# Optimization experiments

Hardware: AMD Instinct MI355X
Metric: run time of the kernel (lower is better)

Reference implementation:

```python
import jax, jax.numpy as jnp
import numpy as np

B, N, D = 4, 1024, 1024
H = 16
DH = D // H  # 64
DROPOUT_P = 0.5


def setup_inputs() -> dict:
    key = jax.random.key(0)
    ks = jax.random.split(key, 6)
    query = jax.random.normal(ks[0], (B, N, D), dtype=jnp.float32)
    key_t = jax.random.normal(ks[1], (B, N, D), dtype=jnp.float32)
    value = jax.random.normal(ks[2], (B, N, D), dtype=jnp.float32)
    # torch Linear(D, 3D): weight [3D, D], bias [3D]
    W_qkv = jax.random.normal(ks[3], (3 * D, D), dtype=jnp.float32) * (1.0 / np.sqrt(D))
    b_qkv = jax.random.normal(ks[4], (3 * D,), dtype=jnp.float32) * 0.01
    # inverted dropout mask: keep_prob = 1 - p, kept entries scaled by 1/keep
    keep = 1.0 - DROPOUT_P
    drop_mask = (jax.random.uniform(ks[5], (B * H, N, N)) < keep).astype(jnp.float32) / keep
    return {"query": query, "key": key_t, "value": value,
            "W_qkv": W_qkv, "b_qkv": b_qkv, "drop_mask": drop_mask}


def _split_heads(t):
    # 'b n (h d) -> (b h) n d'
    b, n, _ = t.shape
    return t.reshape(b, n, H, DH).transpose(0, 2, 1, 3).reshape(b * H, n, DH)


def reference(query, key, value, W_qkv, b_qkv, drop_mask):
    # key/value args are unused by the original module (it derives q,k,v from query)
    qkv = query @ W_qkv.T + b_qkv                      # [b, n, 3d]
    q, k, v = jnp.split(qkv, 3, axis=-1)
    q, k, v = _split_heads(q), _split_heads(k), _split_heads(v)  # [(b h), n, dh]
    qk = jnp.einsum('znd,zmd->znm', q, k)              # [(b h), n, n]
    # faithful quirk: original does qk.div(1/sqrt(dh)) == qk * sqrt(dh)
    scaled_qk = qk * jnp.sqrt(jnp.float32(DH))
    attn = jax.nn.softmax(scaled_qk, axis=-1)
    attn = attn * drop_mask                            # deterministic inverted dropout
    out = jnp.einsum('znm,zmd->znd', attn, v)          # [(b h), n, dh]
    # '(b h) n d -> b n (h d)'
    out = out.reshape(B, H, N, DH).transpose(0, 2, 1, 3).reshape(B, N, D)
    return out
```

## Files before the change

### kernel.cpp

```cpp
#include <hip/hip_runtime.h>


typedef _Float16 f16;
typedef _Float16 f16x4 __attribute__((ext_vector_type(4)));
typedef _Float16 f16x8 __attribute__((ext_vector_type(8)));
typedef float    f32x4 __attribute__((ext_vector_type(4)));

#define MFMA16(a, b, c) __builtin_amdgcn_mfma_f32_16x16x32_f16((a), (b), (c), 0, 0, 0)

__device__ __forceinline__ void gll16(const f16* g, f16* l) {
  __builtin_amdgcn_global_load_lds(
      (const __attribute__((address_space(1))) unsigned int*)g,
      (__attribute__((address_space(3))) unsigned int*)l, 16, 0, 0);
}

__global__ __launch_bounds__(256) void cvt_split(const float4* __restrict__ s,
                                                 f16x4* __restrict__ hi,
                                                 f16x4* __restrict__ lo, int n4) {
  int i = blockIdx.x * 256 + threadIdx.x;
  if (i >= n4) return;
  float4 v = s[i];
  f16x4 h, l;
  h[0] = (f16)v.x; l[0] = (f16)(v.x - (float)h[0]);
  h[1] = (f16)v.y; l[1] = (f16)(v.y - (float)h[1]);
  h[2] = (f16)v.z; l[2] = (f16)(v.z - (float)h[2]);
  h[3] = (f16)v.w; l[3] = (f16)(v.w - (float)h[3]);
  hi[i] = h; lo[i] = l;
}

__global__ __launch_bounds__(256) void proj_gemm(
    const f16* __restrict__ qh, const f16* __restrict__ ql,
    const f16* __restrict__ wh, const f16* __restrict__ wl,
    const float* __restrict__ bias,
    f16* __restrict__ Qh, f16* __restrict__ Ql,
    f16* __restrict__ Kh, f16* __restrict__ Kl,
    f16* __restrict__ Vh) {
  __shared__ f16 As[128 * 32];
  __shared__ f16 Bs[128 * 32];
  const int tid = threadIdx.x;
  const int m0 = blockIdx.y * 128, n0 = blockIdx.x * 128;
  const int wid = tid >> 6, lane = tid & 63;
  const int wm = (wid >> 1) * 64, wn = (wid & 1) * 64;
  const int r16 = lane & 15, g = lane >> 4;

  f32x4 zero4 = {0.f, 0.f, 0.f, 0.f};
  f32x4 acc[4][4];
#pragma unroll
  for (int i = 0; i < 4; ++i)
#pragma unroll
    for (int j = 0; j < 4; ++j) acc[i][j] = zero4;

  const f16* At[3] = {qh, ql, qh};
  const f16* Bt[3] = {wh, wh, wl};
  const int nsteps = (n0 < 2048) ? 96 : 32;

  for (int s = 0; s < nsteps; ++s) {
    const int term = s >> 5, kk = (s & 31) << 5;
    const f16* Ab = At[term] + (size_t)m0 * 1024 + kk;
    const f16* Bb = Bt[term] + (size_t)n0 * 1024 + kk;
#pragma unroll
    for (int it = 0; it < 2; ++it) {
      int c = tid + it * 256;
      int row = c >> 2, cc = c & 3;
      gll16(Ab + row * 1024 + cc * 8, &As[c * 8]);
      gll16(Bb + row * 1024 + cc * 8, &Bs[c * 8]);
    }
    __syncthreads();
    f16x8 a[4], b[4];
#pragma unroll
    for (int i = 0; i < 4; ++i) {
      a[i] = *(const f16x8*)&As[(wm + i * 16 + r16) * 32 + g * 8];
      b[i] = *(const f16x8*)&Bs[(wn + i * 16 + r16) * 32 + g * 8];
    }
#pragma unroll
    for (int i = 0; i < 4; ++i)
#pragma unroll
      for (int j = 0; j < 4; ++j) acc[i][j] = MFMA16(a[i], b[j], acc[i][j]);
    __syncthreads();
  }

#pragma unroll
  for (int j = 0; j < 4; ++j) {
    const int col = n0 + wn + j * 16 + r16;
    const float bv = bias[col];
#pragma unroll
    for (int i = 0; i < 4; ++i) {
#pragma unroll
      for (int rr = 0; rr < 4; ++rr) {
        const int m = m0 + wm + i * 16 + g * 4 + rr;
        const float c = acc[i][j][rr] + bv;
        const int bi = m >> 10, n = m & 1023;
        if (col < 1024) {
          const int z = bi * 16 + (col >> 6), dh = col & 63;
          const size_t idx = ((size_t)z * 1024 + n) * 64 + dh;
          f16 h = (f16)c;
          Qh[idx] = h; Ql[idx] = (f16)(c - (float)h);
        } else if (col < 2048) {
          const int c2 = col - 1024;
          const int z = bi * 16 + (c2 >> 6), dh = c2 & 63;
          const size_t idx = ((size_t)z * 1024 + n) * 64 + dh;
          f16 h = (f16)c;
          Kh[idx] = h; Kl[idx] = (f16)(c - (float)h);
        } else {
          const int c2 = col - 2048;
          const int z = bi * 16 + (c2 >> 6), dh = c2 & 63;
          Vh[((size_t)z * 1024 + n) * 64 + dh] = (f16)c;
        }
      }
    }
  }
}

__global__ __launch_bounds__(256) void transp_v(const f16* __restrict__ Vh,
                                                f16* __restrict__ Vt) {
  __shared__ f16 t[64][80];
  const int z = blockIdx.y, nt = blockIdx.x;
  const int tid = threadIdx.x;
#pragma unroll
  for (int it = 0; it < 2; ++it) {
    int c = tid + it * 256;
    int row = c >> 3, cc = c & 7;
    *(f16x8*)&t[row][cc * 8] =
        *(const f16x8*)&Vh[(((size_t)z << 10) + nt * 64 + row) * 64 + cc * 8];
  }
  __syncthreads();
#pragma unroll
  for (int it = 0; it < 2; ++it) {
    int c = tid + it * 256;
    int dh = c >> 3, ncc = c & 7;
    f16x8 o;
#pragma unroll
    for (int j = 0; j < 8; ++j) o[j] = t[ncc * 8 + j][dh];
    *(f16x8*)&Vt[((size_t)z * 64 + dh) * 1024 + nt * 64 + ncc * 8] = o;
  }
}

__global__ __launch_bounds__(256) void attn(
    const f16* __restrict__ Qh_, const f16* __restrict__ Ql_,
    const f16* __restrict__ Kh_, const f16* __restrict__ Kl_,
    const f16* __restrict__ Vt_, const float* __restrict__ mask,
    float* __restrict__ out) {
  __shared__ f16 Ps[4][1024];

  const int z = blockIdx.y, qt = blockIdx.x;
  const int q0 = qt * 64;
  const int tid = threadIdx.x, w = tid >> 6, lane = tid & 63;
  const int r16 = lane & 15, g = lane >> 4;

  const f16* qrh = Qh_ + ((size_t)z * 1024 + q0 + w * 16 + r16) * 64;
  const f16* qrl = Ql_ + ((size_t)z * 1024 + q0 + w * 16 + r16) * 64;
  f16x8 qa[2], qla[2];
#pragma unroll
  for (int ks = 0; ks < 2; ++ks) {
    qa[ks] = *(const f16x8*)&qrh[ks * 32 + g * 8];
    qla[ks] = *(const f16x8*)&qrl[ks * 32 + g * 8];
  }

  const f16* Kzh = Kh_ + ((size_t)z << 10) * 64;
  const f16* Kzl = Kl_ + ((size_t)z << 10) * 64;
  const f16* Vz = Vt_ + (size_t)z * 64 * 1024;
  const float* mz = mask + ((size_t)z << 20);
  const int qrow_m = q0 + w * 16 + g * 4;

  float mrow[4] = {-1e30f, -1e30f, -1e30f, -1e30f};
  float lrow[4] = {0.f, 0.f, 0.f, 0.f};
  f32x4 zero4 = {0.f, 0.f, 0.f, 0.f};
  f32x4 acc[4];
#pragma unroll
  for (int df = 0; df < 4; ++df) acc[df] = zero4;

  f16* Pw = &Ps[w][0];

  for (int kt = 0; kt < 16; ++kt) {
    const int k0 = kt * 64;

    float mv[4][4];
#pragma unroll
    for (int cf = 0; cf < 4; ++cf)
#pragma unroll
      for (int rr = 0; rr < 4; ++rr)
        mv[cf][rr] = mz[(size_t)(qrow_m + rr) * 1024 + k0 + cf * 16 + r16];

    f32x4 s[4];
#pragma unroll
    for (int cf = 0; cf < 4; ++cf) {
      const f16* kb = Kzh + (size_t)(k0 + cf * 16 + r16) * 64;
      const f16* klb = Kzl + (size_t)(k0 + cf * 16 + r16) * 64;
      f16x8 kh0 = *(const f16x8*)&kb[g * 8];
      f16x8 kh1 = *(const f16x8*)&kb[32 + g * 8];
      f16x8 kl0 = *(const f16x8*)&klb[g * 8];
      f16x8 kl1 = *(const f16x8*)&klb[32 + g * 8];
      f32x4 t = zero4;
      t = MFMA16(qa[0], kh0, t);
      t = MFMA16(qla[0], kh0, t);
      t = MFMA16(qa[0], kl0, t);
      t = MFMA16(qa[1], kh1, t);
      t = MFMA16(qla[1], kh1, t);
      t = MFMA16(qa[1], kl1, t);
      s[cf] = t;
    }

    float s8[4][4];
#pragma unroll
    for (int cf = 0; cf < 4; ++cf)
#pragma unroll
      for (int rr = 0; rr < 4; ++rr) s8[cf][rr] = s[cf][rr] * 8.0f;

    float rm[4];
#pragma unroll
    for (int rr = 0; rr < 4; ++rr)
      rm[rr] = fmaxf(fmaxf(s8[0][rr], s8[1][rr]), fmaxf(s8[2][rr], s8[3][rr]));
#pragma unroll
    for (int mk = 1; mk < 16; mk <<= 1)
#pragma unroll
      for (int rr = 0; rr < 4; ++rr)
        rm[rr] = fmaxf(rm[rr], __shfl_xor(rm[rr], mk, 64));

    float mnew[4], scal[4];
#pragma unroll
    for (int rr = 0; rr < 4; ++rr) {
      mnew[rr] = fmaxf(mrow[rr], rm[rr]);
      scal[rr] = __expf(mrow[rr] - mnew[rr]);
      mrow[rr] = mnew[rr];
    }

    float p_[4][4], rs[4] = {0.f, 0.f, 0.f, 0.f};
#pragma unroll
    for (int cf = 0; cf < 4; ++cf)
#pragma unroll
      for (int rr = 0; rr < 4; ++rr) {
        p_[cf][rr] = __expf(s8[cf][rr] - mnew[rr]);
        rs[rr] += p_[cf][rr];
      }
#pragma unroll
    for (int mk = 1; mk < 16; mk <<= 1)
#pragma unroll
      for (int rr = 0; rr < 4; ++rr) rs[rr] += __shfl_xor(rs[rr], mk, 64);
#pragma unroll
    for (int rr = 0; rr < 4; ++rr) lrow[rr] = lrow[rr] * scal[rr] + rs[rr];
#pragma unroll
    for (int df = 0; df < 4; ++df)
#pragma unroll
      for (int rr = 0; rr < 4; ++rr) acc[df][rr] *= scal[rr];

#pragma unroll
    for (int cf = 0; cf < 4; ++cf)
#pragma unroll
      for (int rr = 0; rr < 4; ++rr) {
        const int prow = g * 4 + rr, key = cf * 16 + r16;
        Pw[prow * 64 + (((key >> 3) ^ (prow & 7)) << 3) + (key & 7)] =
            (f16)(p_[cf][rr] * mv[cf][rr]);
      }
    f16x8 pf[2];
#pragma unroll
    for (int ks2 = 0; ks2 < 2; ++ks2) {
      const int row = r16, c = ks2 * 4 + g;
      pf[ks2] = *(const f16x8*)&Pw[row * 64 + ((c ^ (row & 7)) << 3)];
    }

#pragma unroll
    for (int df = 0; df < 4; ++df) {
      const f16* vb = Vz + (size_t)(df * 16 + r16) * 1024 + k0;
#pragma unroll
      for (int ks2 = 0; ks2 < 2; ++ks2)
        acc[df] =
            MFMA16(pf[ks2], *(const f16x8*)&vb[ks2 * 32 + g * 8], acc[df]);
    }
  }

  const int bi = z >> 4, hh = z & 15;
#pragma unroll
  for (int df = 0; df < 4; ++df)
#pragma unroll
    for (int rr = 0; rr < 4; ++rr) {
      const int n = q0 + w * 16 + g * 4 + rr;
      out[((size_t)bi * 1024 + n) * 1024 + hh * 64 + df * 16 + r16] =
          acc[df][rr] / lrow[rr];
    }
}

extern "C" void kernel_launch(void* const* d_in, const int* in_sizes, int n_in,
                              void* d_out, int out_size, void* d_ws,
                              size_t ws_size, hipStream_t stream) {
  const float* query = (const float*)d_in[0];
  const float* W = (const float*)d_in[3];
  const float* bias = (const float*)d_in[4];
  const float* mask = (const float*)d_in[5];
  float* out = (float*)d_out;

  f16* p = (f16*)d_ws;
  f16* qh = p;              p += (size_t)4096 * 1024;
  f16* ql = p;              p += (size_t)4096 * 1024;
  f16* wh = p;              p += (size_t)3072 * 1024;
  f16* wl = p;              p += (size_t)3072 * 1024;
  f16* Qh = p;              p += (size_t)64 * 1024 * 64;
  f16* Ql = p;              p += (size_t)64 * 1024 * 64;
  f16* Kh = p;              p += (size_t)64 * 1024 * 64;
  f16* Kl = p;              p += (size_t)64 * 1024 * 64;
  f16* Vh = p;              p += (size_t)64 * 1024 * 64;
  f16* Vt = p;

  cvt_split<<<(1048576 + 255) / 256, 256, 0, stream>>>(
      (const float4*)query, (f16x4*)qh, (f16x4*)ql, 1048576);
  cvt_split<<<(786432 + 255) / 256, 256, 0, stream>>>(
      (const float4*)W, (f16x4*)wh, (f16x4*)wl, 786432);
  proj_gemm<<<dim3(24, 32), 256, 0, stream>>>(qh, ql, wh, wl, bias, Qh, Ql, Kh,
                                              Kl, Vh);
  transp_v<<<dim3(16, 64), 256, 0, stream>>>(Vh, Vt);
  attn<<<dim3(16, 64), 256, 0, stream>>>(Qh, Ql, Kh, Kl, Vt, mask, out);
}
```

Before: 648.9 us.

## Stage K/V tiles in LDS with double buffering and fuse split-precision GEMM terms

```diff
diff --git a/kernel.cpp b/kernel.cpp
--- a/kernel.cpp
+++ b/kernel.cpp
@@ -12,6 +12,10 @@
   __builtin_amdgcn_global_load_lds(
       (const __attribute__((address_space(1))) unsigned int*)g,
       (__attribute__((address_space(3))) unsigned int*)l, 16, 0, 0);
+}
+
+__device__ __forceinline__ f16x8 ldsfrag(const f16* tile, int row, int chunk) {
+  return *(const f16x8*)&tile[row * 64 + ((chunk ^ (row & 7)) << 3)];
 }
 
 __global__ __launch_bounds__(256) void cvt_split(const float4* __restrict__ s,
@@ -35,10 +39,12 @@
     f16* __restrict__ Qh, f16* __restrict__ Ql,
     f16* __restrict__ Kh, f16* __restrict__ Kl,
     f16* __restrict__ Vh) {
-  __shared__ f16 As[128 * 32];
-  __shared__ f16 Bs[128 * 32];
+  __shared__ f16 Ah[128 * 32], Al[128 * 32], Bh[128 * 32], Bl[128 * 32];
   const int tid = threadIdx.x;
-  const int m0 = blockIdx.y * 128, n0 = blockIdx.x * 128;
+  const int bid = blockIdx.x;
+  const int wg = (bid & 7) * 96 + (bid >> 3);
+  const int m0 = (wg / 24) * 128, n0 = (wg % 24) * 128;
+  const bool isv = (n0 >= 2048);
   const int wid = tid >> 6, lane = tid & 63;
   const int wm = (wid >> 1) * 64, wn = (wid & 1) * 64;
   const int r16 = lane & 15, g = lane >> 4;
@@ -50,32 +56,46 @@
 #pragma unroll
     for (int j = 0; j < 4; ++j) acc[i][j] = zero4;
 
-  const f16* At[3] = {qh, ql, qh};
-  const f16* Bt[3] = {wh, wh, wl};
-  const int nsteps = (n0 < 2048) ? 96 : 32;
-
-  for (int s = 0; s < nsteps; ++s) {
-    const int term = s >> 5, kk = (s & 31) << 5;
-    const f16* Ab = At[term] + (size_t)m0 * 1024 + kk;
-    const f16* Bb = Bt[term] + (size_t)n0 * 1024 + kk;
+  for (int s = 0; s < 32; ++s) {
+    const int kk = s << 5;
+    const f16* Abh = qh + (size_t)m0 * 1024 + kk;
+    const f16* Abl = ql + (size_t)m0 * 1024 + kk;
+    const f16* Bbh = wh + (size_t)n0 * 1024 + kk;
+    const f16* Bbl = wl + (size_t)n0 * 1024 + kk;
 #pragma unroll
     for (int it = 0; it < 2; ++it) {
-      int c = tid + it * 256;
-      int row = c >> 2, cc = c & 3;
-      gll16(Ab + row * 1024 + cc * 8, &As[c * 8]);
-      gll16(Bb + row * 1024 + cc * 8, &Bs[c * 8]);
+      const int c = tid + it * 256;
+      const int go = (c >> 2) * 1024 + (c & 3) * 8;
+      gll16(Abh + go, &Ah[c * 8]);
+      gll16(Bbh + go, &Bh[c * 8]);
+      if (!isv) {
+        gll16(Abl + go, &Al[c * 8]);
+        gll16(Bbl + go, &Bl[c * 8]);
+      }
     }
     __syncthreads();
-    f16x8 a[4], b[4];
+    f16x8 a[4], al_[4];
 #pragma unroll
     for (int i = 0; i < 4; ++i) {
-      a[i] = *(const f16x8*)&As[(wm + i * 16 + r16) * 32 + g * 8];
-      b[i] = *(const f16x8*)&Bs[(wn + i * 16 + r16) * 32 + g * 8];
-    }
-#pragma unroll
-    for (int i = 0; i < 4; ++i)
-#pragma unroll
-      for (int j = 0; j < 4; ++j) acc[i][j] = MFMA16(a[i], b[j], acc[i][j]);
+      a[i] = *(const f16x8*)&Ah[(wm + i * 16 + r16) * 32 + g * 8];
+      if (!isv) al_[i] = *(const f16x8*)&Al[(wm + i * 16 + r16) * 32 + g * 8];
+    }
+#pragma unroll
+    for (int j = 0; j < 4; ++j) {
+      const f16x8 b = *(const f16x8*)&Bh[(wn + j * 16 + r16) * 32 + g * 8];
+      if (!isv) {
+        const f16x8 bl = *(const f16x8*)&Bl[(wn + j * 16 + r16) * 32 + g * 8];
+#pragma unroll
+        for (int i = 0; i < 4; ++i) {
+          acc[i][j] = MFMA16(a[i], b, acc[i][j]);
+          acc[i][j] = MFMA16(al_[i], b, acc[i][j]);
+          acc[i][j] = MFMA16(a[i], bl, acc[i][j]);
+        }
+      } else {
+#pragma unroll
+        for (int i = 0; i < 4; ++i) acc[i][j] = MFMA16(a[i], b, acc[i][j]);
+      }
+    }
     __syncthreads();
   }
 
@@ -135,20 +155,24 @@
   }
 }
 
-__global__ __launch_bounds__(256) void attn(
+__global__ __launch_bounds__(512) void attn(
     const f16* __restrict__ Qh_, const f16* __restrict__ Ql_,
     const f16* __restrict__ Kh_, const f16* __restrict__ Kl_,
     const f16* __restrict__ Vt_, const float* __restrict__ mask,
     float* __restrict__ out) {
-  __shared__ f16 Ps[4][1024];
-
-  const int z = blockIdx.y, qt = blockIdx.x;
-  const int q0 = qt * 64;
+  __shared__ f16 Khs[2][4096], Kls[2][4096], Vts[2][4096];
+  __shared__ f16 Ps[8][1024];
+
+  const int bid = blockIdx.x;
+  const int wg = (bid & 7) * 64 + (bid >> 3);
+  const int qt = wg & 7, z = wg >> 3;
+  const int q0 = qt * 128;
   const int tid = threadIdx.x, w = tid >> 6, lane = tid & 63;
   const int r16 = lane & 15, g = lane >> 4;
 
-  const f16* qrh = Qh_ + ((size_t)z * 1024 + q0 + w * 16 + r16) * 64;
-  const f16* qrl = Ql_ + ((size_t)z * 1024 + q0 + w * 16 + r16) * 64;
+  const size_t zrow = (size_t)z << 10;
+  const f16* qrh = Qh_ + (zrow + q0 + w * 16 + r16) * 64;
+  const f16* qrl = Ql_ + (zrow + q0 + w * 16 + r16) * 64;
   f16x8 qa[2], qla[2];
 #pragma unroll
   for (int ks = 0; ks < 2; ++ks) {
@@ -156,11 +180,19 @@
     qla[ks] = *(const f16x8*)&qrl[ks * 32 + g * 8];
   }
 
-  const f16* Kzh = Kh_ + ((size_t)z << 10) * 64;
-  const f16* Kzl = Kl_ + ((size_t)z << 10) * 64;
-  const f16* Vz = Vt_ + (size_t)z * 64 * 1024;
-  const float* mz = mask + ((size_t)z << 20);
-  const int qrow_m = q0 + w * 16 + g * 4;
+  const f16* KzhB = Kh_ + zrow * 64;
+  const f16* KzlB = Kl_ + zrow * 64;
+  const f16* VzB = Vt_ + (size_t)z * 64 * 1024;
+  const int sc = tid, srow = sc >> 3, ssc = ((sc & 7) ^ (srow & 7)) << 3;
+
+#define STAGE(buf, k0_)                                                   \
+  do {                                                                    \
+    gll16(KzhB + (size_t)((k0_) + srow) * 64 + ssc, &Khs[buf][sc * 8]);   \
+    gll16(KzlB + (size_t)((k0_) + srow) * 64 + ssc, &Kls[buf][sc * 8]);   \
+    gll16(VzB + (size_t)srow * 1024 + (k0_) + ssc, &Vts[buf][sc * 8]);    \
+  } while (0)
+
+  STAGE(0, 0);
 
   float mrow[4] = {-1e30f, -1e30f, -1e30f, -1e30f};
   float lrow[4] = {0.f, 0.f, 0.f, 0.f};
@@ -169,10 +201,15 @@
 #pragma unroll
   for (int df = 0; df < 4; ++df) acc[df] = zero4;
 
+  const float* mz = mask + ((size_t)z << 20);
+  const int qrow_m = q0 + w * 16 + g * 4;
   f16* Pw = &Ps[w][0];
+  __syncthreads();
 
   for (int kt = 0; kt < 16; ++kt) {
-    const int k0 = kt * 64;
+    const int cur = kt & 1;
+    const int k0 = kt << 6;
+    if (kt < 15) STAGE(cur ^ 1, k0 + 64);
 
     float mv[4][4];
 #pragma unroll
@@ -181,15 +218,15 @@
       for (int rr = 0; rr < 4; ++rr)
         mv[cf][rr] = mz[(size_t)(qrow_m + rr) * 1024 + k0 + cf * 16 + r16];
 
+    __builtin_amdgcn_s_setprio(1);
     f32x4 s[4];
 #pragma unroll
     for (int cf = 0; cf < 4; ++cf) {
-      const f16* kb = Kzh + (size_t)(k0 + cf * 16 + r16) * 64;
-      const f16* klb = Kzl + (size_t)(k0 + cf * 16 + r16) * 64;
-      f16x8 kh0 = *(const f16x8*)&kb[g * 8];
-      f16x8 kh1 = *(const f16x8*)&kb[32 + g * 8];
-      f16x8 kl0 = *(const f16x8*)&klb[g * 8];
-      f16x8 kl1 = *(const f16x8*)&klb[32 + g * 8];
+      const int krow = cf * 16 + r16;
+      const f16x8 kh0 = ldsfrag(&Khs[cur][0], krow, g);
+      const f16x8 kh1 = ldsfrag(&Khs[cur][0], krow, 4 + g);
+      const f16x8 kl0 = ldsfrag(&Kls[cur][0], krow, g);
+      const f16x8 kl1 = ldsfrag(&Kls[cur][0], krow, 4 + g);
       f32x4 t = zero4;
       t = MFMA16(qa[0], kh0, t);
       t = MFMA16(qla[0], kh0, t);
@@ -199,6 +236,7 @@
       t = MFMA16(qa[1], kl1, t);
       s[cf] = t;
     }
+    __builtin_amdgcn_s_setprio(0);
 
     float s8[4][4];
 #pragma unroll
@@ -253,19 +291,19 @@
       }
     f16x8 pf[2];
 #pragma unroll
-    for (int ks2 = 0; ks2 < 2; ++ks2) {
-      const int row = r16, c = ks2 * 4 + g;
-      pf[ks2] = *(const f16x8*)&Pw[row * 64 + ((c ^ (row & 7)) << 3)];
-    }
-
-#pragma unroll
-    for (int df = 0; df < 4; ++df) {
-      const f16* vb = Vz + (size_t)(df * 16 + r16) * 1024 + k0;
+    for (int ks2 = 0; ks2 < 2; ++ks2)
+      pf[ks2] = ldsfrag(Pw, r16, ks2 * 4 + g);
+
+    __builtin_amdgcn_s_setprio(1);
+#pragma unroll
+    for (int df = 0; df < 4; ++df)
 #pragma unroll
       for (int ks2 = 0; ks2 < 2; ++ks2)
-        acc[df] =
-            MFMA16(pf[ks2], *(const f16x8*)&vb[ks2 * 32 + g * 8], acc[df]);
-    }
+        acc[df] = MFMA16(pf[ks2],
+                         ldsfrag(&Vts[cur][0], df * 16 + r16, ks2 * 4 + g),
+                         acc[df]);
+    __builtin_amdgcn_s_setprio(0);
+    __syncthreads();
   }
 
   const int bi = z >> 4, hh = z & 15;
@@ -277,6 +315,7 @@
       out[((size_t)bi * 1024 + n) * 1024 + hh * 64 + df * 16 + r16] =
           acc[df][rr] / lrow[rr];
     }
+#undef STAGE
 }
 
 extern "C" void kernel_launch(void* const* d_in, const int* in_sizes, int n_in,
@@ -304,8 +343,7 @@
       (const float4*)query, (f16x4*)qh, (f16x4*)ql, 1048576);
   cvt_split<<<(786432 + 255) / 256, 256, 0, stream>>>(
       (const float4*)W, (f16x4*)wh, (f16x4*)wl, 786432);
-  proj_gemm<<<dim3(24, 32), 256, 0, stream>>>(qh, ql, wh, wl, bias, Qh, Ql, Kh,
-                                              Kl, Vh);
+  proj_gemm<<<768, 256, 0, stream>>>(qh, ql, wh, wl, bias, Qh, Ql, Kh, Kl, Vh);
   transp_v<<<dim3(16, 64), 256, 0, stream>>>(Vh, Vt);
-  attn<<<dim3(16, 64), 256, 0, stream>>>(Qh, Ql, Kh, Kl, Vt, mask, out);
-}
+  attn<<<512, 512, 0, stream>>>(Qh, Ql, Kh, Kl, Vt, mask, out);
+}
```

New measurement: 561.8 us. -13.4%, faster.
